# Performance work log

Measured on AMD Instinct MI355X. Metric: run time of the kernel, lower is better.

Reference implementation:

```python
import jax, jax.numpy as jnp
import numpy as np


def setup_inputs() -> dict:
    key = jax.random.key(0)
    ks = jax.random.split(key, 12)
    N, E, G = 100000, 1000000, 64
    D = 64            # node/edge/global feature dim
    IN = 4 * D        # concat: edge + receiver + sender + global = 256
    H, OUT = 128, 128 # latent_sizes, n_feat_out
    x = jax.random.normal(ks[0], (N, D), dtype=jnp.float32)
    e = jax.random.normal(ks[1], (E, D), dtype=jnp.float32)
    u = jax.random.normal(ks[2], (G, D), dtype=jnp.float32)
    edge_index = jax.random.randint(ks[3], (2, E), 0, N, dtype=jnp.int64)
    batch = jnp.sort(jax.random.randint(ks[4], (N,), 0, G, dtype=jnp.int64))
    s1 = 1.0 / np.sqrt(IN)
    s2 = 1.0 / np.sqrt(H)
    W1 = jax.random.uniform(ks[5], (IN, H), minval=-s1, maxval=s1, dtype=jnp.float32)
    b1 = jax.random.uniform(ks[6], (H,), minval=-s1, maxval=s1, dtype=jnp.float32)
    W2 = jax.random.uniform(ks[7], (H, OUT), minval=-s2, maxval=s2, dtype=jnp.float32)
    b2 = jax.random.uniform(ks[8], (OUT,), minval=-s2, maxval=s2, dtype=jnp.float32)
    ln_g = jnp.ones((OUT,), dtype=jnp.float32)
    ln_b = jnp.zeros((OUT,), dtype=jnp.float32)
    return {"x": x, "e": e, "u": u, "W1": W1, "b1": b1, "W2": W2, "b2": b2,
            "ln_g": ln_g, "ln_b": ln_b, "edge_index": edge_index, "batch": batch}


def _layernorm(h, g, b, eps=1e-5):
    mu = jnp.mean(h, axis=-1, keepdims=True)
    var = jnp.mean(jnp.square(h - mu), axis=-1, keepdims=True)
    return (h - mu) * jax.lax.rsqrt(var + eps) * g + b


def reference(x, e, u, W1, b1, W2, b2, ln_g, ln_b, edge_index, batch):
    row, col = edge_index[0], edge_index[1]
    sender = x[row]                    # [E, D]
    receiver = x[col]                  # [E, D]
    glob = u[batch[row]]               # globals scattered to edges [E, D]
    attrs = jnp.concatenate([e, receiver, sender, glob], axis=1)  # [E, 4D]
    h = jax.nn.relu(attrs @ W1 + b1)   # hidden layer
    h = jax.nn.relu(h @ W2 + b2)       # activate_final=True
    out = _layernorm(h, ln_g, ln_b)    # normalize=True
    return out
```

## Files before the change

### kernel.cpp

```cpp
#include <hip/hip_runtime.h>

typedef __bf16 bf16_t;
typedef __bf16 bf16x8 __attribute__((ext_vector_type(8)));
typedef float  f32x4  __attribute__((ext_vector_type(4)));
typedef unsigned short u16;

__device__ __forceinline__ u16 f2bf(float f) {
    union { float f; unsigned u; } v; v.f = f;
    unsigned u = v.u;
    return (u16)((u + 0x7fffu + ((u >> 16) & 1u)) >> 16);
}

__global__ __launch_bounds__(256) void prep_weights(
    const float* __restrict__ W1, const float* __restrict__ W2,
    u16* __restrict__ W1t, u16* __restrict__ W2t)
{
    int tid = blockIdx.x * 256 + threadIdx.x;
    if (tid < 128 * 256) {
        int n = tid >> 8, k = tid & 255;
        W1t[tid] = f2bf(W1[k * 128 + n]);
    } else if (tid < 128 * 256 + 128 * 128) {
        int t = tid - 128 * 256;
        int n = t >> 7, k = t & 127;
        W2t[t] = f2bf(W2[k * 128 + n]);
    }
}

__global__ __launch_bounds__(256) void prep_cast(
    const float* __restrict__ x, const float* __restrict__ u,
    bf16_t* __restrict__ xb, bf16_t* __restrict__ ub, int nx, int nu)
{
    int total = (nx + nu) >> 2;
    for (int i = blockIdx.x * 256 + threadIdx.x; i < total; i += gridDim.x * 256) {
        int j = i << 2;
        const float* src; bf16_t* dst;
        if (j < nx) { src = x + j;        dst = xb + j; }
        else        { src = u + (j - nx); dst = ub + (j - nx); }
        float4 v = *(const float4*)src;
        dst[0] = (__bf16)v.x; dst[1] = (__bf16)v.y;
        dst[2] = (__bf16)v.z; dst[3] = (__bf16)v.w;
    }
}

__device__ __forceinline__ bf16x8 cvt8(const float* __restrict__ p) {
    float4 a = *(const float4*)p;
    float4 b = *(const float4*)(p + 4);
    bf16x8 r;
    r[0] = (__bf16)a.x; r[1] = (__bf16)a.y; r[2] = (__bf16)a.z; r[3] = (__bf16)a.w;
    r[4] = (__bf16)b.x; r[5] = (__bf16)b.y; r[6] = (__bf16)b.z; r[7] = (__bf16)b.w;
    return r;
}

template<bool PRECAST>
__global__ __launch_bounds__(256, 4) void edge_mlp(
    const float* __restrict__ x, const float* __restrict__ e, const float* __restrict__ u,
    const bf16_t* __restrict__ xb, const bf16_t* __restrict__ ub,
    const float* __restrict__ b1, const float* __restrict__ b2,
    const float* __restrict__ ln_g, const float* __restrict__ ln_b,
    const int* __restrict__ edge_index, const int* __restrict__ batch,
    const bf16_t* __restrict__ W1t, const bf16_t* __restrict__ W2t,
    float* __restrict__ out, int E)
{
    __shared__ __align__(16) u16 sH[4][32 * 128];

    const int wave = threadIdx.x >> 6;
    const int lane = threadIdx.x & 63;
    const int lrow = lane & 15;
    const int kg   = lane >> 4;
    const int lk   = kg * 8;

    const long tb = (long)(blockIdx.x * 4 + wave) * 32;
    if (tb >= E) return;

    const int eid0 = (int)tb + lrow;
    const int eid1 = eid0 + 16;
    const int r0 = edge_index[eid0],     r1 = edge_index[eid1];
    const int c0 = edge_index[E + eid0], c1 = edge_index[E + eid1];
    const int g0 = batch[r0],            g1 = batch[r1];

    const float*  ep0 = e + (size_t)eid0 * 64;
    const float*  ep1 = e + (size_t)eid1 * 64;

    f32x4 acc[2][8] = {};

    const bf16_t* w1b = W1t + lrow * 256 + lk;

    #pragma unroll
    for (int kk = 0; kk < 8; ++kk) {
        const int off = (kk & 1) * 32 + lk;
        bf16x8 a0, a1;
        if (kk < 2) {
            a0 = cvt8(ep0 + off);
            a1 = cvt8(ep1 + off);
        } else if (kk < 4) {
            if (PRECAST) {
                a0 = *(const bf16x8*)(xb + (size_t)c0 * 64 + off);
                a1 = *(const bf16x8*)(xb + (size_t)c1 * 64 + off);
            } else {
                a0 = cvt8(x + (size_t)c0 * 64 + off);
                a1 = cvt8(x + (size_t)c1 * 64 + off);
            }
        } else if (kk < 6) {
            if (PRECAST) {
                a0 = *(const bf16x8*)(xb + (size_t)r0 * 64 + off);
                a1 = *(const bf16x8*)(xb + (size_t)r1 * 64 + off);
            } else {
                a0 = cvt8(x + (size_t)r0 * 64 + off);
                a1 = cvt8(x + (size_t)r1 * 64 + off);
            }
        } else {
            if (PRECAST) {
                a0 = *(const bf16x8*)(ub + (size_t)g0 * 64 + off);
                a1 = *(const bf16x8*)(ub + (size_t)g1 * 64 + off);
            } else {
                a0 = cvt8(u + (size_t)g0 * 64 + off);
                a1 = cvt8(u + (size_t)g1 * 64 + off);
            }
        }
        #pragma unroll
        for (int n = 0; n < 8; ++n) {
            bf16x8 b = *(const bf16x8*)(w1b + n * 16 * 256 + kk * 32);
            acc[0][n] = __builtin_amdgcn_mfma_f32_16x16x32_bf16(a0, b, acc[0][n], 0, 0, 0);
            acc[1][n] = __builtin_amdgcn_mfma_f32_16x16x32_bf16(a1, b, acc[1][n], 0, 0, 0);
        }
    }

    float bias1[8];
    #pragma unroll
    for (int n = 0; n < 8; ++n) bias1[n] = b1[n * 16 + lrow];

    u16* hb = sH[wave];
    #pragma unroll
    for (int m = 0; m < 2; ++m)
        #pragma unroll
        for (int n = 0; n < 8; ++n)
            #pragma unroll
            for (int r = 0; r < 4; ++r) {
                float v = acc[m][n][r] + bias1[n];
                v = v > 0.f ? v : 0.f;
                int row = m * 16 + kg * 4 + r;
                int bo  = row * 256 + (n * 16 + lrow) * 2;
                bo ^= (row & 7) << 4;
                *(u16*)((char*)hb + bo) = __builtin_bit_cast(u16, (__bf16)v);
            }

    asm volatile("s_waitcnt lgkmcnt(0)" ::: "memory");
    __builtin_amdgcn_sched_barrier(0);

    f32x4 acc2[2][8] = {};
    const bf16_t* w2b = W2t + lrow * 128 + lk;

    #pragma unroll
    for (int kk = 0; kk < 4; ++kk) {
        bf16x8 a0, a1;
        {
            int row = lrow;
            int bo  = row * 256 + (kk * 32 + lk) * 2;
            bo ^= (row & 7) << 4;
            a0 = *(const bf16x8*)((const char*)hb + bo);
        }
        {
            int row = 16 + lrow;
            int bo  = row * 256 + (kk * 32 + lk) * 2;
            bo ^= (row & 7) << 4;
            a1 = *(const bf16x8*)((const char*)hb + bo);
        }
        #pragma unroll
        for (int n = 0; n < 8; ++n) {
            bf16x8 b = *(const bf16x8*)(w2b + n * 16 * 128 + kk * 32);
            acc2[0][n] = __builtin_amdgcn_mfma_f32_16x16x32_bf16(a0, b, acc2[0][n], 0, 0, 0);
            acc2[1][n] = __builtin_amdgcn_mfma_f32_16x16x32_bf16(a1, b, acc2[1][n], 0, 0, 0);
        }
    }

    float bias2[8], gg[8], bb[8];
    #pragma unroll
    for (int n = 0; n < 8; ++n) {
        bias2[n] = b2[n * 16 + lrow];
        gg[n]    = ln_g[n * 16 + lrow];
        bb[n]    = ln_b[n * 16 + lrow];
    }

    #pragma unroll
    for (int m = 0; m < 2; ++m)
        #pragma unroll
        for (int n = 0; n < 8; ++n)
            #pragma unroll
            for (int r = 0; r < 4; ++r) {
                float t = acc2[m][n][r] + bias2[n];
                acc2[m][n][r] = t > 0.f ? t : 0.f;
            }

    #pragma unroll
    for (int m = 0; m < 2; ++m)
        #pragma unroll
        for (int r = 0; r < 4; ++r) {
            float s = 0.f, s2 = 0.f;
            #pragma unroll
            for (int n = 0; n < 8; ++n) {
                float v = acc2[m][n][r];
                s += v; s2 += v * v;
            }
            #pragma unroll
            for (int msk = 1; msk < 16; msk <<= 1) {
                s  += __shfl_xor(s,  msk, 64);
                s2 += __shfl_xor(s2, msk, 64);
            }
            float mu   = s * (1.f / 128.f);
            float var  = s2 * (1.f / 128.f) - mu * mu;
            float rstd = rsqrtf(var + 1e-5f);

            long edge = tb + m * 16 + kg * 4 + r;
            float* orow = out + (size_t)edge * 128;
            #pragma unroll
            for (int n = 0; n < 8; ++n)
                orow[n * 16 + lrow] = (acc2[m][n][r] - mu) * rstd * gg[n] + bb[n];
        }
}

extern "C" void kernel_launch(void* const* d_in, const int* in_sizes, int n_in,
                              void* d_out, int out_size, void* d_ws, size_t ws_size,
                              hipStream_t stream) {
    const float* x    = (const float*)d_in[0];
    const float* e    = (const float*)d_in[1];
    const float* u    = (const float*)d_in[2];
    const float* W1   = (const float*)d_in[3];
    const float* b1   = (const float*)d_in[4];
    const float* W2   = (const float*)d_in[5];
    const float* b2   = (const float*)d_in[6];
    const float* ln_g = (const float*)d_in[7];
    const float* ln_b = (const float*)d_in[8];
    const int*   edge_index = (const int*)d_in[9];
    const int*   batch      = (const int*)d_in[10];

    const int E  = in_sizes[9] / 2;
    const int nx = in_sizes[0];
    const int nu = in_sizes[2];

    u16* W1t = (u16*)d_ws;
    u16* W2t = W1t + 128 * 256;
    bf16_t* xbp = (bf16_t*)(W2t + 128 * 128);
    bf16_t* ubp = xbp + nx;

    size_t needed = 98304 + (size_t)(nx + nu) * 2;
    bool precast = ws_size >= needed;

    prep_weights<<<192, 256, 0, stream>>>(W1, W2, W1t, W2t);

    int nblk = (E + 127) / 128;
    if (precast) {
        int cgrid = ((nx + nu) / 4 + 255) / 256;
        if (cgrid > 2048) cgrid = 2048;
        prep_cast<<<cgrid, 256, 0, stream>>>(x, u, xbp, ubp, nx, nu);
        edge_mlp<true><<<nblk, 256, 0, stream>>>(x, e, u, xbp, ubp, b1, b2, ln_g, ln_b,
                                                 edge_index, batch,
                                                 (const bf16_t*)W1t, (const bf16_t*)W2t,
                                                 (float*)d_out, E);
    } else {
        edge_mlp<false><<<nblk, 256, 0, stream>>>(x, e, u, nullptr, nullptr, b1, b2, ln_g, ln_b,
                                                  edge_index, batch,
                                                  (const bf16_t*)W1t, (const bf16_t*)W2t,
                                                  (float*)d_out, E);
    }
}
```

Measured before the change: 1.077 ms.

## Persistent edge MLP with LDS-resident weights, register-shuffled hidden, prefetched gathers

Replaces the one-tile-per-wave kernel with a persistent 256-block, 1024-thread kernel. Each block stages both bf16 weight matrices and the bias and layernorm parameters in LDS once. Waves loop over 16-edge tiles and prefetch the next tile's gathered features while computing the current one. The MFMA operands are swapped so the hidden layer can pass from the first GEMM to the second through cross-lane shuffles instead of an LDS round-trip, and outputs are written as float4. A separate pre-pass packs row, column and graph index per edge to cut dependent index loads, at the cost of an extra kernel and workspace traffic. Large LDS use (about 98KB) and 1024-thread blocks limit occupancy, and the launch_bounds(1024,4) request looks unattainable.

```diff
diff --git a/kernel.cpp b/kernel.cpp
--- a/kernel.cpp
+++ b/kernel.cpp
@@ -4,11 +4,30 @@
 typedef __bf16 bf16x8 __attribute__((ext_vector_type(8)));
 typedef float  f32x4  __attribute__((ext_vector_type(4)));
 typedef unsigned short u16;
+typedef unsigned int   u32;
+
+union BF8 { bf16x8 v; uint4 w; };
+struct Frag8 { bf16x8 f[8]; };
 
 __device__ __forceinline__ u16 f2bf(float f) {
     union { float f; unsigned u; } v; v.f = f;
     unsigned u = v.u;
     return (u16)((u + 0x7fffu + ((u >> 16) & 1u)) >> 16);
+}
+
+__device__ __forceinline__ u32 pk(float lo, float hi) {
+    u16 a = __builtin_bit_cast(u16, (__bf16)lo);
+    u16 b = __builtin_bit_cast(u16, (__bf16)hi);
+    return (u32)a | ((u32)b << 16);
+}
+
+__device__ __forceinline__ bf16x8 cvt8(const float* __restrict__ p) {
+    float4 a = *(const float4*)p;
+    float4 b = *(const float4*)(p + 4);
+    bf16x8 r;
+    r[0] = (__bf16)a.x; r[1] = (__bf16)a.y; r[2] = (__bf16)a.z; r[3] = (__bf16)a.w;
+    r[4] = (__bf16)b.x; r[5] = (__bf16)b.y; r[6] = (__bf16)b.z; r[7] = (__bf16)b.w;
+    return r;
 }
 
 __global__ __launch_bounds__(256) void prep_weights(
@@ -42,180 +61,193 @@
     }
 }
 
-__device__ __forceinline__ bf16x8 cvt8(const float* __restrict__ p) {
-    float4 a = *(const float4*)p;
-    float4 b = *(const float4*)(p + 4);
-    bf16x8 r;
-    r[0] = (__bf16)a.x; r[1] = (__bf16)a.y; r[2] = (__bf16)a.z; r[3] = (__bf16)a.w;
-    r[4] = (__bf16)b.x; r[5] = (__bf16)b.y; r[6] = (__bf16)b.z; r[7] = (__bf16)b.w;
-    return r;
-}
-
-template<bool PRECAST>
-__global__ __launch_bounds__(256, 4) void edge_mlp(
+__global__ __launch_bounds__(256) void prep_rcg(
+    const int* __restrict__ ei, const int* __restrict__ batch,
+    int4* __restrict__ rcg, int E)
+{
+    int i = blockIdx.x * 256 + threadIdx.x;
+    if (i < E) {
+        int r = ei[i], c = ei[E + i];
+        rcg[i] = make_int4(r, c, batch[r], 0);
+    }
+}
+
+template<int MODE>
+__global__ __launch_bounds__(1024, 4) void edge_mlp(
     const float* __restrict__ x, const float* __restrict__ e, const float* __restrict__ u,
     const bf16_t* __restrict__ xb, const bf16_t* __restrict__ ub,
     const float* __restrict__ b1, const float* __restrict__ b2,
     const float* __restrict__ ln_g, const float* __restrict__ ln_b,
-    const int* __restrict__ edge_index, const int* __restrict__ batch,
-    const bf16_t* __restrict__ W1t, const bf16_t* __restrict__ W2t,
+    const int* __restrict__ ei, const int* __restrict__ batch,
+    const int4* __restrict__ rcg,
+    const u16* __restrict__ W1t, const u16* __restrict__ W2t,
     float* __restrict__ out, int E)
 {
-    __shared__ __align__(16) u16 sH[4][32 * 128];
-
-    const int wave = threadIdx.x >> 6;
-    const int lane = threadIdx.x & 63;
-    const int lrow = lane & 15;
-    const int kg   = lane >> 4;
-    const int lk   = kg * 8;
-
-    const long tb = (long)(blockIdx.x * 4 + wave) * 32;
-    if (tb >= E) return;
-
-    const int eid0 = (int)tb + lrow;
-    const int eid1 = eid0 + 16;
-    const int r0 = edge_index[eid0],     r1 = edge_index[eid1];
-    const int c0 = edge_index[E + eid0], c1 = edge_index[E + eid1];
-    const int g0 = batch[r0],            g1 = batch[r1];
-
-    const float*  ep0 = e + (size_t)eid0 * 64;
-    const float*  ep1 = e + (size_t)eid1 * 64;
-
-    f32x4 acc[2][8] = {};
-
-    const bf16_t* w1b = W1t + lrow * 256 + lk;
-
+    __shared__ __align__(16) u16 sW1[128 * 256];
+    __shared__ __align__(16) u16 sW2[128 * 128];
+    __shared__ __align__(16) float sP[512];
+
+    const int tid = threadIdx.x;
     #pragma unroll
-    for (int kk = 0; kk < 8; ++kk) {
-        const int off = (kk & 1) * 32 + lk;
-        bf16x8 a0, a1;
-        if (kk < 2) {
-            a0 = cvt8(ep0 + off);
-            a1 = cvt8(ep1 + off);
-        } else if (kk < 4) {
-            if (PRECAST) {
-                a0 = *(const bf16x8*)(xb + (size_t)c0 * 64 + off);
-                a1 = *(const bf16x8*)(xb + (size_t)c1 * 64 + off);
+    for (int i = 0; i < 4; ++i) {
+        int byte = (i * 1024 + tid) * 16;
+        int row  = byte >> 9;
+        *(uint4*)((char*)sW1 + (byte ^ ((row & 7) << 4))) =
+            *(const uint4*)((const char*)W1t + byte);
+    }
+    #pragma unroll
+    for (int i = 0; i < 2; ++i) {
+        int byte = (i * 1024 + tid) * 16;
+        int row  = byte >> 8;
+        *(uint4*)((char*)sW2 + (byte ^ ((row & 7) << 4))) =
+            *(const uint4*)((const char*)W2t + byte);
+    }
+    if (tid < 128) {
+        sP[tid]       = b1[tid];   sP[128 + tid] = b2[tid];
+        sP[256 + tid] = ln_g[tid]; sP[384 + tid] = ln_b[tid];
+    }
+    __syncthreads();
+
+    const int wave = tid >> 6, lane = tid & 63;
+    const int lrow = lane & 15, kg = lane >> 4;
+    const int swz  = (lrow & 7) << 4;
+    const int NT = (E + 15) >> 4;
+    const int STRIDE = gridDim.x * 16;
+    int wt = blockIdx.x * 16 + wave;
+    if (wt >= NT) return;
+
+    auto ldidx = [&](int t) -> int4 {
+        int eid = t * 16 + lrow; eid = eid < E ? eid : E - 1;
+        if constexpr (MODE == 2) { int4 r = rcg[eid]; r.w = eid; return r; }
+        else {
+            int4 r; r.x = ei[eid]; r.y = ei[E + eid]; r.z = batch[r.x]; r.w = eid;
+            return r;
+        }
+    };
+    auto gather = [&](int4 ix) -> Frag8 {
+        Frag8 g;
+        const float* ep = e + (size_t)ix.w * 64;
+        #pragma unroll
+        for (int q = 0; q < 2; ++q) {
+            int off = q * 32 + kg * 8;
+            g.f[q] = cvt8(ep + off);
+            if constexpr (MODE >= 1) {
+                g.f[2 + q] = *(const bf16x8*)(xb + (size_t)ix.y * 64 + off);
+                g.f[4 + q] = *(const bf16x8*)(xb + (size_t)ix.x * 64 + off);
+                g.f[6 + q] = *(const bf16x8*)(ub + (size_t)ix.z * 64 + off);
             } else {
-                a0 = cvt8(x + (size_t)c0 * 64 + off);
-                a1 = cvt8(x + (size_t)c1 * 64 + off);
-            }
-        } else if (kk < 6) {
-            if (PRECAST) {
-                a0 = *(const bf16x8*)(xb + (size_t)r0 * 64 + off);
-                a1 = *(const bf16x8*)(xb + (size_t)r1 * 64 + off);
-            } else {
-                a0 = cvt8(x + (size_t)r0 * 64 + off);
-                a1 = cvt8(x + (size_t)r1 * 64 + off);
-            }
-        } else {
-            if (PRECAST) {
-                a0 = *(const bf16x8*)(ub + (size_t)g0 * 64 + off);
-                a1 = *(const bf16x8*)(ub + (size_t)g1 * 64 + off);
-            } else {
-                a0 = cvt8(u + (size_t)g0 * 64 + off);
-                a1 = cvt8(u + (size_t)g1 * 64 + off);
-            }
-        }
-        #pragma unroll
-        for (int n = 0; n < 8; ++n) {
-            bf16x8 b = *(const bf16x8*)(w1b + n * 16 * 256 + kk * 32);
-            acc[0][n] = __builtin_amdgcn_mfma_f32_16x16x32_bf16(a0, b, acc[0][n], 0, 0, 0);
-            acc[1][n] = __builtin_amdgcn_mfma_f32_16x16x32_bf16(a1, b, acc[1][n], 0, 0, 0);
-        }
-    }
-
-    float bias1[8];
-    #pragma unroll
-    for (int n = 0; n < 8; ++n) bias1[n] = b1[n * 16 + lrow];
-
-    u16* hb = sH[wave];
-    #pragma unroll
-    for (int m = 0; m < 2; ++m)
-        #pragma unroll
-        for (int n = 0; n < 8; ++n)
+                g.f[2 + q] = cvt8(x + (size_t)ix.y * 64 + off);
+                g.f[4 + q] = cvt8(x + (size_t)ix.x * 64 + off);
+                g.f[6 + q] = cvt8(u + (size_t)ix.z * 64 + off);
+            }
+        }
+        return g;
+    };
+
+    int4  iN = ldidx(wt);
+    Frag8 g  = gather(iN);
+    {
+        int nwt = wt + STRIDE; nwt = nwt < NT ? nwt : wt;
+        iN = ldidx(nwt);
+    }
+
+    for (; wt < NT; wt += STRIDE) {
+        const long tb = (long)wt * 16;
+
+        f32x4 a1[8] = {};
+        #pragma unroll
+        for (int kk = 0; kk < 8; ++kk) {
+            #pragma unroll
+            for (int mt = 0; mt < 8; ++mt) {
+                int byte = ((mt * 16 + lrow) << 9) + (kk << 6) + (kg << 4);
+                bf16x8 wf = *(const bf16x8*)((const char*)sW1 + (byte ^ swz));
+                a1[mt] = __builtin_amdgcn_mfma_f32_16x16x32_bf16(wf, g.f[kk], a1[mt], 0, 0, 0);
+            }
+        }
+
+        #pragma unroll
+        for (int mt = 0; mt < 8; ++mt) {
+            float4 bv = *(const float4*)(sP + mt * 16 + kg * 4);
             #pragma unroll
             for (int r = 0; r < 4; ++r) {
-                float v = acc[m][n][r] + bias1[n];
+                float v = a1[mt][r] + (&bv.x)[r];
+                a1[mt][r] = v > 0.f ? v : 0.f;
+            }
+        }
+
+        const int src_lo = ((kg & 1) * 2) * 16 + lrow;
+        const int src_hi = src_lo + 16;
+        const bool hi = kg >= 2;
+        bf16x8 pfr[4];
+        #pragma unroll
+        for (int kk = 0; kk < 4; ++kk) {
+            u32 A0 = pk(a1[kk * 2][0],     a1[kk * 2][1]);
+            u32 A1 = pk(a1[kk * 2][2],     a1[kk * 2][3]);
+            u32 B0 = pk(a1[kk * 2 + 1][0], a1[kk * 2 + 1][1]);
+            u32 B1 = pk(a1[kk * 2 + 1][2], a1[kk * 2 + 1][3]);
+            u32 tA0 = (u32)__shfl((int)A0, src_lo, 64);
+            u32 tA1 = (u32)__shfl((int)A1, src_lo, 64);
+            u32 tA2 = (u32)__shfl((int)A0, src_hi, 64);
+            u32 tA3 = (u32)__shfl((int)A1, src_hi, 64);
+            u32 tB0 = (u32)__shfl((int)B0, src_lo, 64);
+            u32 tB1 = (u32)__shfl((int)B1, src_lo, 64);
+            u32 tB2 = (u32)__shfl((int)B0, src_hi, 64);
+            u32 tB3 = (u32)__shfl((int)B1, src_hi, 64);
+            BF8 t;
+            t.w = make_uint4(hi ? tB0 : tA0, hi ? tB1 : tA1,
+                             hi ? tB2 : tA2, hi ? tB3 : tA3);
+            pfr[kk] = t.v;
+        }
+
+        g = gather(iN);
+        {
+            int nwt = wt + 2 * STRIDE; nwt = nwt < NT ? nwt : wt;
+            iN = ldidx(nwt);
+        }
+
+        f32x4 a2[8] = {};
+        #pragma unroll
+        for (int kk = 0; kk < 4; ++kk) {
+            #pragma unroll
+            for (int mt = 0; mt < 8; ++mt) {
+                int byte = ((mt * 16 + lrow) << 8) + (kk << 6) + (kg << 4);
+                bf16x8 wf = *(const bf16x8*)((const char*)sW2 + (byte ^ swz));
+                a2[mt] = __builtin_amdgcn_mfma_f32_16x16x32_bf16(wf, pfr[kk], a2[mt], 0, 0, 0);
+            }
+        }
+
+        float s = 0.f, s2 = 0.f;
+        #pragma unroll
+        for (int mt = 0; mt < 8; ++mt) {
+            float4 bv = *(const float4*)(sP + 128 + mt * 16 + kg * 4);
+            #pragma unroll
+            for (int r = 0; r < 4; ++r) {
+                float v = a2[mt][r] + (&bv.x)[r];
                 v = v > 0.f ? v : 0.f;
-                int row = m * 16 + kg * 4 + r;
-                int bo  = row * 256 + (n * 16 + lrow) * 2;
-                bo ^= (row & 7) << 4;
-                *(u16*)((char*)hb + bo) = __builtin_bit_cast(u16, (__bf16)v);
-            }
-
-    asm volatile("s_waitcnt lgkmcnt(0)" ::: "memory");
-    __builtin_amdgcn_sched_barrier(0);
-
-    f32x4 acc2[2][8] = {};
-    const bf16_t* w2b = W2t + lrow * 128 + lk;
-
-    #pragma unroll
-    for (int kk = 0; kk < 4; ++kk) {
-        bf16x8 a0, a1;
-        {
-            int row = lrow;
-            int bo  = row * 256 + (kk * 32 + lk) * 2;
-            bo ^= (row & 7) << 4;
-            a0 = *(const bf16x8*)((const char*)hb + bo);
-        }
-        {
-            int row = 16 + lrow;
-            int bo  = row * 256 + (kk * 32 + lk) * 2;
-            bo ^= (row & 7) << 4;
-            a1 = *(const bf16x8*)((const char*)hb + bo);
-        }
-        #pragma unroll
-        for (int n = 0; n < 8; ++n) {
-            bf16x8 b = *(const bf16x8*)(w2b + n * 16 * 128 + kk * 32);
-            acc2[0][n] = __builtin_amdgcn_mfma_f32_16x16x32_bf16(a0, b, acc2[0][n], 0, 0, 0);
-            acc2[1][n] = __builtin_amdgcn_mfma_f32_16x16x32_bf16(a1, b, acc2[1][n], 0, 0, 0);
-        }
-    }
-
-    float bias2[8], gg[8], bb[8];
-    #pragma unroll
-    for (int n = 0; n < 8; ++n) {
-        bias2[n] = b2[n * 16 + lrow];
-        gg[n]    = ln_g[n * 16 + lrow];
-        bb[n]    = ln_b[n * 16 + lrow];
-    }
-
-    #pragma unroll
-    for (int m = 0; m < 2; ++m)
-        #pragma unroll
-        for (int n = 0; n < 8; ++n)
-            #pragma unroll
-            for (int r = 0; r < 4; ++r) {
-                float t = acc2[m][n][r] + bias2[n];
-                acc2[m][n][r] = t > 0.f ? t : 0.f;
-            }
-
-    #pragma unroll
-    for (int m = 0; m < 2; ++m)
-        #pragma unroll
-        for (int r = 0; r < 4; ++r) {
-            float s = 0.f, s2 = 0.f;
-            #pragma unroll
-            for (int n = 0; n < 8; ++n) {
-                float v = acc2[m][n][r];
-                s += v; s2 += v * v;
-            }
-            #pragma unroll
-            for (int msk = 1; msk < 16; msk <<= 1) {
-                s  += __shfl_xor(s,  msk, 64);
-                s2 += __shfl_xor(s2, msk, 64);
-            }
-            float mu   = s * (1.f / 128.f);
-            float var  = s2 * (1.f / 128.f) - mu * mu;
-            float rstd = rsqrtf(var + 1e-5f);
-
-            long edge = tb + m * 16 + kg * 4 + r;
+                a2[mt][r] = v; s += v; s2 += v * v;
+            }
+        }
+        s  += __shfl_xor(s, 16, 64);  s  += __shfl_xor(s, 32, 64);
+        s2 += __shfl_xor(s2, 16, 64); s2 += __shfl_xor(s2, 32, 64);
+        float mu   = s * (1.f / 128.f);
+        float rstd = rsqrtf(s2 * (1.f / 128.f) - mu * mu + 1e-5f);
+
+        long edge = tb + lrow;
+        if (edge < E) {
             float* orow = out + (size_t)edge * 128;
             #pragma unroll
-            for (int n = 0; n < 8; ++n)
-                orow[n * 16 + lrow] = (acc2[m][n][r] - mu) * rstd * gg[n] + bb[n];
-        }
+            for (int mt = 0; mt < 8; ++mt) {
+                float4 gv = *(const float4*)(sP + 256 + mt * 16 + kg * 4);
+                float4 bv = *(const float4*)(sP + 384 + mt * 16 + kg * 4);
+                float4 o;
+                o.x = (a2[mt][0] - mu) * rstd * gv.x + bv.x;
+                o.y = (a2[mt][1] - mu) * rstd * gv.y + bv.y;
+                o.z = (a2[mt][2] - mu) * rstd * gv.z + bv.z;
+                o.w = (a2[mt][3] - mu) * rstd * gv.w + bv.w;
+                *(float4*)(orow + mt * 16 + kg * 4) = o;
+            }
+        }
+    }
 }
 
 extern "C" void kernel_launch(void* const* d_in, const int* in_sizes, int n_in,
@@ -230,8 +262,8 @@
     const float* b2   = (const float*)d_in[6];
     const float* ln_g = (const float*)d_in[7];
     const float* ln_b = (const float*)d_in[8];
-    const int*   edge_index = (const int*)d_in[9];
-    const int*   batch      = (const int*)d_in[10];
+    const int*   ei   = (const int*)d_in[9];
+    const int*   batch= (const int*)d_in[10];
 
     const int E  = in_sizes[9] / 2;
     const int nx = in_sizes[0];
@@ -241,25 +273,36 @@
     u16* W2t = W1t + 128 * 256;
     bf16_t* xbp = (bf16_t*)(W2t + 128 * 128);
     bf16_t* ubp = xbp + nx;
-
-    size_t needed = 98304 + (size_t)(nx + nu) * 2;
-    bool precast = ws_size >= needed;
+    unsigned long long rp = (unsigned long long)(ubp + nu);
+    rp = (rp + 15ull) & ~15ull;
+    int4* rcg = (int4*)rp;
+
+    const size_t base = 98304;
+    const size_t xu   = (size_t)(nx + nu) * 2;
+    int mode = 0;
+    if      (ws_size >= base + xu + 16 + (size_t)E * 16) mode = 2;
+    else if (ws_size >= base + xu)                       mode = 1;
 
     prep_weights<<<192, 256, 0, stream>>>(W1, W2, W1t, W2t);
-
-    int nblk = (E + 127) / 128;
-    if (precast) {
+    if (mode >= 1) {
         int cgrid = ((nx + nu) / 4 + 255) / 256;
         if (cgrid > 2048) cgrid = 2048;
         prep_cast<<<cgrid, 256, 0, stream>>>(x, u, xbp, ubp, nx, nu);
-        edge_mlp<true><<<nblk, 256, 0, stream>>>(x, e, u, xbp, ubp, b1, b2, ln_g, ln_b,
-                                                 edge_index, batch,
-                                                 (const bf16_t*)W1t, (const bf16_t*)W2t,
-                                                 (float*)d_out, E);
-    } else {
-        edge_mlp<false><<<nblk, 256, 0, stream>>>(x, e, u, nullptr, nullptr, b1, b2, ln_g, ln_b,
-                                                  edge_index, batch,
-                                                  (const bf16_t*)W1t, (const bf16_t*)W2t,
-                                                  (float*)d_out, E);
-    }
-}
+    }
+    if (mode == 2)
+        prep_rcg<<<(E + 255) / 256, 256, 0, stream>>>(ei, batch, rcg, E);
+
+    dim3 grid(256), blk(1024);
+    if (mode == 2)
+        edge_mlp<2><<<grid, blk, 0, stream>>>(x, e, u, xbp, ubp, b1, b2, ln_g, ln_b,
+                                              ei, batch, rcg,
+                                              W1t, W2t, (float*)d_out, E);
+    else if (mode == 1)
+        edge_mlp<1><<<grid, blk, 0, stream>>>(x, e, u, xbp, ubp, b1, b2, ln_g, ln_b,
+                                              ei, batch, nullptr,
+                                              W1t, W2t, (float*)d_out, E);
+    else
+        edge_mlp<0><<<grid, blk, 0, stream>>>(x, e, u, nullptr, nullptr, b1, b2, ln_g, ln_b,
+                                              ei, batch, nullptr,
+                                              W1t, W2t, (float*)d_out, E);
+}
```

Result: slower. 2.437 ms (+126.3%).
